# Performance work log

Hardware: AMD Instinct MI355X
Metric: run time of the kernel (lower is better)

Reference implementation:

```python
import jax, jax.numpy as jnp
import numpy as np
import math


def _build_lookup(S):
    # Vectorized port of build_hierarchical_index_lookup_table (static, numpy).
    L = int(math.log2(S))
    total = 2 * S - 1
    max_valid = total - 2  # root is never a neighbor
    idx = np.full((S, L), -1, dtype=np.int32)
    cmask = np.zeros((S, L), dtype=bool)
    n = np.arange(S, dtype=np.int64)
    for lvl in range(L):
        if lvl == 0:
            nn = n ^ 1
            pair = n
        else:
            pair = n // 2 + S
            nn = pair ^ 1
        valid = nn <= max_valid
        idx[:, lvl] = np.where(valid, nn.astype(np.int32), idx[:, lvl])
        cmask[:, lvl] = np.where(valid, (pair < nn) & valid, cmask[:, lvl])
        n = nn
    return jnp.asarray(idx), jnp.asarray(cmask)


def _tree_kv(k, v, levels, scale):
    # Build parent nodes bottom-up. Parent K is the mean of its two children;
    # parent V is refined by the fused parent-self attention (build_parent_nodes):
    # 3-way softmax over [self, child0, child1] with eps 1e-9 in the denominator.
    K_parts, V_parts = [k], [v]
    Kc, Vc = k, v
    for _ in range(levels):
        Kc0, Kc1 = Kc[:, 0::2], Kc[:, 1::2]
        Vc0, Vc1 = Vc[:, 0::2], Vc[:, 1::2]
        Kp = 0.5 * (Kc0 + Kc1)
        Vp = 0.5 * (Vc0 + Vc1)
        s_self = jnp.einsum('bphd,bphd->bph', Kp, Kp) * scale
        s0 = jnp.einsum('bphd,bphd->bph', Kp, Kc0) * scale
        s1 = jnp.einsum('bphd,bphd->bph', Kp, Kc1) * scale
        m = jnp.maximum(s_self, jnp.maximum(s0, s1))
        e_self = jnp.exp(s_self - m)
        e0 = jnp.exp(s0 - m)
        e1 = jnp.exp(s1 - m)
        denom = e_self + e0 + e1 + 1e-9
        Vp = (e_self[..., None] * Vp + e0[..., None] * Vc0 + e1[..., None] * Vc1) / denom[..., None]
        K_parts.append(Kp)
        V_parts.append(Vp)
        Kc, Vc = Kp, Vp
    # Full tree: leaves first, then each parent level -> [B, 2S-1, H, D]
    return jnp.concatenate(K_parts, axis=1), jnp.concatenate(V_parts, axis=1)


def setup_inputs() -> dict:
    key = jax.random.key(0)
    kq, kk, kv = jax.random.split(key, 3)
    B, S, H, D = 4, 4096, 8, 64
    q = jax.random.normal(kq, (B, S, H, D), dtype=jnp.float32)
    k = jax.random.normal(kk, (B, S, H, D), dtype=jnp.float32)
    v = jax.random.normal(kv, (B, S, H, D), dtype=jnp.float32)
    return {'q': q, 'k': k, 'v': v}


def reference(q, k, v):
    B, S, H, D = q.shape
    L = int(math.log2(S))
    scale = 1.0 / math.sqrt(D)
    idx, cmask = _build_lookup(S)          # [S, L] int32, [S, L] bool
    Kf, Vf = _tree_kv(k, v, L, scale)      # [B, 2S-1, H, D]
    kc = Kf[:, idx]                        # [B, S, L, H, D] tree-indexed gather
    vc = Vf[:, idx]
    s_self = jnp.einsum('bshd,bshd->bsh', q, k) * scale
    s_cross = jnp.einsum('bshd,bslhd->bshl', q, kc) * scale
    s_cross = jnp.where(cmask[None, :, None, :], -jnp.inf, s_cross)
    m = jnp.maximum(s_self, jnp.max(s_cross, axis=-1))  # online-softmax max
    e_self = jnp.exp(s_self - m)
    e_cross = jnp.exp(s_cross - m[..., None])
    denom = e_self + jnp.sum(e_cross, axis=-1)
    out = (e_self[..., None] * v + jnp.einsum('bshl,bslhd->bshd', e_cross, vc)) / denom[..., None]
    return out
```

## Files before the change

### kernel.cpp

```cpp
#include <hip/hip_runtime.h>


#define S 4096
#define H 8
#define D 64
#define B 4
#define NINT 4094
#define NBH 32
#define SCALE 0.125f

__device__ inline float red16(float x) {
    x += __shfl_xor(x, 1);
    x += __shfl_xor(x, 2);
    x += __shfl_xor(x, 4);
    x += __shfl_xor(x, 8);
    return x;
}

__device__ inline float dot4(const float4 a, const float4 b) {
    return a.x * b.x + a.y * b.y + a.z * b.z + a.w * b.w;
}

__device__ inline void combine(const float4 k0, const float4 k1,
                               const float4 v0, const float4 v1,
                               float4& kp, float4& vp) {
    kp.x = 0.5f * (k0.x + k1.x);
    kp.y = 0.5f * (k0.y + k1.y);
    kp.z = 0.5f * (k0.z + k1.z);
    kp.w = 0.5f * (k0.w + k1.w);
    float pss = red16(dot4(kp, kp)) * SCALE;
    float p0  = red16(dot4(kp, k0)) * SCALE;
    float p1  = red16(dot4(kp, k1)) * SCALE;
    float m  = fmaxf(pss, fmaxf(p0, p1));
    float es = __expf(pss - m), e0 = __expf(p0 - m), e1 = __expf(p1 - m);
    float inv = 1.0f / (es + e0 + e1 + 1e-9f);
    float h = 0.5f * es;
    vp.x = ((h + e0) * v0.x + (h + e1) * v1.x) * inv;
    vp.y = ((h + e0) * v0.y + (h + e1) * v1.y) * inv;
    vp.z = ((h + e0) * v0.z + (h + e1) * v1.z) * inv;
    vp.w = ((h + e0) * v0.w + (h + e1) * v1.w) * inv;
}

__global__ __launch_bounds__(256) void tree_chunk(
    const float* __restrict__ k, const float* __restrict__ v,
    float* __restrict__ kt, float* __restrict__ vt)
{
    __shared__ float lkA[32 * 64], lvA[32 * 64];
    __shared__ float lkB[16 * 64], lvB[16 * 64];
    const int t = threadIdx.x;
    const int sub = t & 15;
    const int pg = t >> 4;
    const int blk = blockIdx.x;
    const int c = blk & 63;
    const int bh = blk >> 6;
    const int b = bh >> 3, h = bh & 7;

#pragma unroll
    for (int r = 0; r < 2; ++r) {
        int j = pg + r * 16;
        int s0 = c * 64 + 2 * j;
        size_t a0 = ((((size_t)b * S + s0) * H + h) * D) + sub * 4;
        float4 k0 = *(const float4*)(k + a0);
        float4 k1 = *(const float4*)(k + a0 + H * D);
        float4 v0 = *(const float4*)(v + a0);
        float4 v1 = *(const float4*)(v + a0 + H * D);
        float4 kp, vp;
        combine(k0, k1, v0, v1, kp, vp);
        *(float4*)(lkA + j * 64 + sub * 4) = kp;
        *(float4*)(lvA + j * 64 + sub * 4) = vp;
        size_t g = ((size_t)bh * NINT + c * 32 + j) * 64 + sub * 4;
        *(float4*)(kt + g) = kp;
        *(float4*)(vt + g) = vp;
    }
    __syncthreads();

    float *sk = lkA, *sv = lvA, *dk = lkB, *dv = lvB;
#pragma unroll
    for (int l = 2; l <= 6; ++l) {
        int np = 64 >> l;
        int goff = S - (S >> (l - 1));
        if (pg < np) {
            int j = pg;
            float4 k0 = *(const float4*)(sk + (2 * j) * 64 + sub * 4);
            float4 k1 = *(const float4*)(sk + (2 * j + 1) * 64 + sub * 4);
            float4 v0 = *(const float4*)(sv + (2 * j) * 64 + sub * 4);
            float4 v1 = *(const float4*)(sv + (2 * j + 1) * 64 + sub * 4);
            float4 kp, vp;
            combine(k0, k1, v0, v1, kp, vp);
            if (l < 6) {
                *(float4*)(dk + j * 64 + sub * 4) = kp;
                *(float4*)(dv + j * 64 + sub * 4) = vp;
            }
            size_t g = ((size_t)bh * NINT + goff + c * np + j) * 64 + sub * 4;
            *(float4*)(kt + g) = kp;
            *(float4*)(vt + g) = vp;
        }
        __syncthreads();
        float* tp;
        tp = sk; sk = dk; dk = tp;
        tp = sv; sv = dv; dv = tp;
    }
}

__global__ __launch_bounds__(256) void tree_top(
    float* __restrict__ kt, float* __restrict__ vt)
{
    __shared__ float lkA[64 * 64], lvA[64 * 64];
    __shared__ float lkB[32 * 64], lvB[32 * 64];
    const int t = threadIdx.x;
    const int sub = t & 15;
    const int pg = t >> 4;
    const int bh = blockIdx.x;

    for (int i = t; i < 1024; i += 256) {
        size_t g = ((size_t)bh * NINT + 3968) * 64 + i * 4;
        *(float4*)(lkA + i * 4) = *(const float4*)(kt + g);
        *(float4*)(lvA + i * 4) = *(const float4*)(vt + g);
    }
    __syncthreads();

    float *sk = lkA, *sv = lvA, *dk = lkB, *dv = lvB;
    int cn = 64;
#pragma unroll
    for (int l = 7; l <= 11; ++l) {
        int np = cn >> 1;
        int goff = S - (S >> (l - 1));
        for (int j = pg; j < np; j += 16) {
            float4 k0 = *(const float4*)(sk + (2 * j) * 64 + sub * 4);
            float4 k1 = *(const float4*)(sk + (2 * j + 1) * 64 + sub * 4);
            float4 v0 = *(const float4*)(sv + (2 * j) * 64 + sub * 4);
            float4 v1 = *(const float4*)(sv + (2 * j + 1) * 64 + sub * 4);
            float4 kp, vp;
            combine(k0, k1, v0, v1, kp, vp);
            if (l < 11) {
                *(float4*)(dk + j * 64 + sub * 4) = kp;
                *(float4*)(dv + j * 64 + sub * 4) = vp;
            }
            size_t g = ((size_t)bh * NINT + goff + j) * 64 + sub * 4;
            *(float4*)(kt + g) = kp;
            *(float4*)(vt + g) = vp;
        }
        __syncthreads();
        float* tp;
        tp = sk; sk = dk; dk = tp;
        tp = sv; sv = dv; dv = tp;
        cn = np;
    }
}

__global__ __launch_bounds__(256) void attn(
    const float* __restrict__ q, const float* __restrict__ k,
    const float* __restrict__ v,
    const float* __restrict__ kt, const float* __restrict__ vt,
    float* __restrict__ out)
{
    int t = blockIdx.x * 256 + threadIdx.x;
    int lane = t & 63;
    int sub = lane & 15;
    int qi = lane >> 4;
    int w = t >> 6;
    int hg = w & 1;
    int s = (w >> 1) & (S - 1);
    int b = w >> 13;
    int h = hg * 4 + qi;
    int bh = b * 8 + h;
    size_t qa = ((((size_t)b * S + s) * H + h) * D) + sub * 4;

    float4 q4 = *(const float4*)(q + qa);
    float4 k4 = *(const float4*)(k + qa);
    float4 v4 = *(const float4*)(v + qa);

    float4 kc[12], vc[12];
    size_t tb = (size_t)bh * NINT;
#pragma unroll
    for (int l = 0; l < 12; ++l) {
        if ((s >> l) & 1) {
            if (l == 0) {
                kc[0] = *(const float4*)(k + qa - H * D);
                vc[0] = *(const float4*)(v + qa - H * D);
            } else {
                int node = (S - (S >> (l - 1))) + ((s >> l) ^ 1);
                size_t a = (tb + node) * 64 + sub * 4;
                kc[l] = *(const float4*)(kt + a);
                vc[l] = *(const float4*)(vt + a);
            }
        }
    }

    float ss = red16(dot4(q4, k4)) * SCALE;
    float sc[12];
#pragma unroll
    for (int l = 0; l < 12; ++l) {
        if ((s >> l) & 1) sc[l] = red16(dot4(q4, kc[l])) * SCALE;
        else              sc[l] = -1e38f;
    }

    float m = ss;
#pragma unroll
    for (int l = 0; l < 12; ++l) m = fmaxf(m, sc[l]);

    float es = __expf(ss - m);
    float denom = es;
    float4 acc;
    acc.x = es * v4.x; acc.y = es * v4.y; acc.z = es * v4.z; acc.w = es * v4.w;
#pragma unroll
    for (int l = 0; l < 12; ++l) {
        if ((s >> l) & 1) {
            float e = __expf(sc[l] - m);
            denom += e;
            acc.x += e * vc[l].x;
            acc.y += e * vc[l].y;
            acc.z += e * vc[l].z;
            acc.w += e * vc[l].w;
        }
    }
    float inv = 1.0f / denom;
    float4 o;
    o.x = acc.x * inv; o.y = acc.y * inv; o.z = acc.z * inv; o.w = acc.w * inv;
    *(float4*)(out + qa) = o;
}

extern "C" void kernel_launch(void* const* d_in, const int* in_sizes, int n_in,
                              void* d_out, int out_size, void* d_ws, size_t ws_size,
                              hipStream_t stream) {
    const float* q = (const float*)d_in[0];
    const float* k = (const float*)d_in[1];
    const float* v = (const float*)d_in[2];
    float* outp = (float*)d_out;
    float* kt = (float*)d_ws;
    float* vt = kt + (size_t)NBH * NINT * D;

    hipLaunchKernelGGL(tree_chunk, dim3(NBH * 64), dim3(256), 0, stream,
                       k, v, kt, vt);
    hipLaunchKernelGGL(tree_top, dim3(NBH), dim3(256), 0, stream, kt, vt);
    hipLaunchKernelGGL(attn, dim3((B * S * 2 * 64) / 256), dim3(256), 0, stream,
                       q, k, v, kt, vt, outp);
}
```

Measured before the change: 177.0 us.

## Recompute low tree levels in attention chunks, store only upper levels globally

```diff
diff --git a/kernel.cpp b/kernel.cpp
--- a/kernel.cpp
+++ b/kernel.cpp
@@ -5,8 +5,8 @@
 #define H 8
 #define D 64
 #define B 4
-#define NINT 4094
 #define NBH 32
+#define NHI 126
 #define SCALE 0.125f
 
 __device__ inline float red16(float x) {
@@ -41,9 +41,9 @@
     vp.w = ((h + e0) * v0.w + (h + e1) * v1.w) * inv;
 }
 
-__global__ __launch_bounds__(256) void tree_chunk(
+__global__ __launch_bounds__(256) void chunk_root(
     const float* __restrict__ k, const float* __restrict__ v,
-    float* __restrict__ kt, float* __restrict__ vt)
+    float* __restrict__ khi, float* __restrict__ vhi)
 {
     __shared__ float lkA[32 * 64], lvA[32 * 64];
     __shared__ float lkB[16 * 64], lvB[16 * 64];
@@ -68,9 +68,6 @@
         combine(k0, k1, v0, v1, kp, vp);
         *(float4*)(lkA + j * 64 + sub * 4) = kp;
         *(float4*)(lvA + j * 64 + sub * 4) = vp;
-        size_t g = ((size_t)bh * NINT + c * 32 + j) * 64 + sub * 4;
-        *(float4*)(kt + g) = kp;
-        *(float4*)(vt + g) = vp;
     }
     __syncthreads();
 
@@ -78,7 +75,6 @@
 #pragma unroll
     for (int l = 2; l <= 6; ++l) {
         int np = 64 >> l;
-        int goff = S - (S >> (l - 1));
         if (pg < np) {
             int j = pg;
             float4 k0 = *(const float4*)(sk + (2 * j) * 64 + sub * 4);
@@ -90,10 +86,11 @@
             if (l < 6) {
                 *(float4*)(dk + j * 64 + sub * 4) = kp;
                 *(float4*)(dv + j * 64 + sub * 4) = vp;
-            }
-            size_t g = ((size_t)bh * NINT + goff + c * np + j) * 64 + sub * 4;
-            *(float4*)(kt + g) = kp;
-            *(float4*)(vt + g) = vp;
+            } else {
+                size_t g = ((size_t)bh * NHI + c) * 64 + sub * 4;
+                *(float4*)(khi + g) = kp;
+                *(float4*)(vhi + g) = vp;
+            }
         }
         __syncthreads();
         float* tp;
@@ -102,122 +99,186 @@
     }
 }
 
-__global__ __launch_bounds__(256) void tree_top(
-    float* __restrict__ kt, float* __restrict__ vt)
+__global__ __launch_bounds__(256) void build_hi(
+    float* __restrict__ khi, float* __restrict__ vhi)
 {
-    __shared__ float lkA[64 * 64], lvA[64 * 64];
-    __shared__ float lkB[32 * 64], lvB[32 * 64];
+    __shared__ float lk[NHI * 64], lv[NHI * 64];
     const int t = threadIdx.x;
     const int sub = t & 15;
     const int pg = t >> 4;
     const int bh = blockIdx.x;
+    size_t base = (size_t)bh * NHI * 64;
 
     for (int i = t; i < 1024; i += 256) {
-        size_t g = ((size_t)bh * NINT + 3968) * 64 + i * 4;
-        *(float4*)(lkA + i * 4) = *(const float4*)(kt + g);
-        *(float4*)(lvA + i * 4) = *(const float4*)(vt + g);
+        *(float4*)(lk + i * 4) = *(const float4*)(khi + base + i * 4);
+        *(float4*)(lv + i * 4) = *(const float4*)(vhi + base + i * 4);
     }
     __syncthreads();
 
-    float *sk = lkA, *sv = lvA, *dk = lkB, *dv = lvB;
-    int cn = 64;
+    int srcOff = 0, dstOff = 64, np = 32;
 #pragma unroll
     for (int l = 7; l <= 11; ++l) {
-        int np = cn >> 1;
-        int goff = S - (S >> (l - 1));
         for (int j = pg; j < np; j += 16) {
-            float4 k0 = *(const float4*)(sk + (2 * j) * 64 + sub * 4);
-            float4 k1 = *(const float4*)(sk + (2 * j + 1) * 64 + sub * 4);
-            float4 v0 = *(const float4*)(sv + (2 * j) * 64 + sub * 4);
-            float4 v1 = *(const float4*)(sv + (2 * j + 1) * 64 + sub * 4);
+            float4 k0 = *(const float4*)(lk + (srcOff + 2 * j) * 64 + sub * 4);
+            float4 k1 = *(const float4*)(lk + (srcOff + 2 * j + 1) * 64 + sub * 4);
+            float4 v0 = *(const float4*)(lv + (srcOff + 2 * j) * 64 + sub * 4);
+            float4 v1 = *(const float4*)(lv + (srcOff + 2 * j + 1) * 64 + sub * 4);
             float4 kp, vp;
             combine(k0, k1, v0, v1, kp, vp);
-            if (l < 11) {
-                *(float4*)(dk + j * 64 + sub * 4) = kp;
-                *(float4*)(dv + j * 64 + sub * 4) = vp;
-            }
-            size_t g = ((size_t)bh * NINT + goff + j) * 64 + sub * 4;
-            *(float4*)(kt + g) = kp;
-            *(float4*)(vt + g) = vp;
+            *(float4*)(lk + (dstOff + j) * 64 + sub * 4) = kp;
+            *(float4*)(lv + (dstOff + j) * 64 + sub * 4) = vp;
+            *(float4*)(khi + base + (size_t)(dstOff + j) * 64 + sub * 4) = kp;
+            *(float4*)(vhi + base + (size_t)(dstOff + j) * 64 + sub * 4) = vp;
         }
         __syncthreads();
-        float* tp;
-        tp = sk; sk = dk; dk = tp;
-        tp = sv; sv = dv; dv = tp;
-        cn = np;
-    }
-}
-
-__global__ __launch_bounds__(256) void attn(
+        srcOff = dstOff; dstOff += np; np >>= 1;
+    }
+}
+
+__global__ __launch_bounds__(256) void attn_chunk(
     const float* __restrict__ q, const float* __restrict__ k,
     const float* __restrict__ v,
-    const float* __restrict__ kt, const float* __restrict__ vt,
+    const float* __restrict__ khi, const float* __restrict__ vhi,
     float* __restrict__ out)
 {
-    int t = blockIdx.x * 256 + threadIdx.x;
-    int lane = t & 63;
-    int sub = lane & 15;
-    int qi = lane >> 4;
-    int w = t >> 6;
-    int hg = w & 1;
-    int s = (w >> 1) & (S - 1);
-    int b = w >> 13;
-    int h = hg * 4 + qi;
-    int bh = b * 8 + h;
-    size_t qa = ((((size_t)b * S + s) * H + h) * D) + sub * 4;
-
-    float4 q4 = *(const float4*)(q + qa);
-    float4 k4 = *(const float4*)(k + qa);
-    float4 v4 = *(const float4*)(v + qa);
-
-    float4 kc[12], vc[12];
-    size_t tb = (size_t)bh * NINT;
-#pragma unroll
-    for (int l = 0; l < 12; ++l) {
-        if ((s >> l) & 1) {
-            if (l == 0) {
-                kc[0] = *(const float4*)(k + qa - H * D);
-                vc[0] = *(const float4*)(v + qa - H * D);
-            } else {
-                int node = (S - (S >> (l - 1))) + ((s >> l) ^ 1);
-                size_t a = (tb + node) * 64 + sub * 4;
-                kc[l] = *(const float4*)(kt + a);
-                vc[l] = *(const float4*)(vt + a);
-            }
-        }
-    }
-
-    float ss = red16(dot4(q4, k4)) * SCALE;
-    float sc[12];
-#pragma unroll
-    for (int l = 0; l < 12; ++l) {
-        if ((s >> l) & 1) sc[l] = red16(dot4(q4, kc[l])) * SCALE;
-        else              sc[l] = -1e38f;
-    }
-
-    float m = ss;
-#pragma unroll
-    for (int l = 0; l < 12; ++l) m = fmaxf(m, sc[l]);
-
-    float es = __expf(ss - m);
-    float denom = es;
-    float4 acc;
-    acc.x = es * v4.x; acc.y = es * v4.y; acc.z = es * v4.z; acc.w = es * v4.w;
-#pragma unroll
-    for (int l = 0; l < 12; ++l) {
-        if ((s >> l) & 1) {
-            float e = __expf(sc[l] - m);
+    __shared__ float tk[62 * 64], tv[62 * 64];
+    __shared__ float pk[6 * 64], pv[6 * 64];
+    const int t = threadIdx.x;
+    const int sub = t & 15;
+    const int pg = t >> 4;
+    const int blk = blockIdx.x;
+    const int c = blk & 63;
+    const int bh = blk >> 6;
+    const int b = bh >> 3, h = bh & 7;
+
+    if (pg < 12) {
+        int lh = (pg >= 6) ? pg - 6 : pg;
+        if ((c >> lh) & 1) {
+            int off = 128 - (128 >> lh);
+            int node = off + ((c >> lh) ^ 1);
+            size_t a = ((size_t)bh * NHI + node) * 64 + sub * 4;
+            if (pg < 6) *(float4*)(pk + lh * 64 + sub * 4) = *(const float4*)(khi + a);
+            else        *(float4*)(pv + lh * 64 + sub * 4) = *(const float4*)(vhi + a);
+        }
+    }
+
+#pragma unroll
+    for (int r = 0; r < 2; ++r) {
+        int j = pg + r * 16;
+        int s0 = c * 64 + 2 * j;
+        size_t a0 = ((((size_t)b * S + s0) * H + h) * D) + sub * 4;
+        float4 k0 = *(const float4*)(k + a0);
+        float4 k1 = *(const float4*)(k + a0 + H * D);
+        float4 v0 = *(const float4*)(v + a0);
+        float4 v1 = *(const float4*)(v + a0 + H * D);
+        float4 kp, vp;
+        combine(k0, k1, v0, v1, kp, vp);
+        *(float4*)(tk + j * 64 + sub * 4) = kp;
+        *(float4*)(tv + j * 64 + sub * 4) = vp;
+    }
+    __syncthreads();
+
+    {
+        int srcOff = 0, dstOff = 32, np = 16;
+#pragma unroll
+        for (int l = 2; l <= 5; ++l) {
+            if (pg < np) {
+                int j = pg;
+                float4 k0 = *(const float4*)(tk + (srcOff + 2 * j) * 64 + sub * 4);
+                float4 k1 = *(const float4*)(tk + (srcOff + 2 * j + 1) * 64 + sub * 4);
+                float4 v0 = *(const float4*)(tv + (srcOff + 2 * j) * 64 + sub * 4);
+                float4 v1 = *(const float4*)(tv + (srcOff + 2 * j + 1) * 64 + sub * 4);
+                float4 kp, vp;
+                combine(k0, k1, v0, v1, kp, vp);
+                *(float4*)(tk + (dstOff + j) * 64 + sub * 4) = kp;
+                *(float4*)(tv + (dstOff + j) * 64 + sub * 4) = vp;
+            }
+            __syncthreads();
+            srcOff = dstOff; dstOff += np; np >>= 1;
+        }
+    }
+
+#pragma unroll 1
+    for (int r = 0; r < 4; ++r) {
+        int sl = pg + r * 16;
+        int s = c * 64 + sl;
+        size_t qa = ((((size_t)b * S + s) * H + h) * D) + sub * 4;
+        float4 q4 = *(const float4*)(q + qa);
+        float4 k4 = *(const float4*)(k + qa);
+        float4 v4 = *(const float4*)(v + qa);
+
+        float ss = red16(dot4(q4, k4)) * SCALE;
+
+        float sc[12];
+        float4 vc0 = v4;
+        const bool odd = (s & 1) != 0;
+        if (odd) {
+            float4 kc0 = *(const float4*)(k + qa - H * D);
+            vc0 = *(const float4*)(v + qa - H * D);
+            sc[0] = red16(dot4(q4, kc0)) * SCALE;
+        } else {
+            sc[0] = -1e38f;
+        }
+#pragma unroll
+        for (int l = 1; l <= 5; ++l) {
+            if ((s >> l) & 1) {
+                int base = 64 - (64 >> (l - 1));
+                int loc = base + (((s >> l) ^ 1) - (c << (6 - l)));
+                float4 kc = *(const float4*)(tk + loc * 64 + sub * 4);
+                sc[l] = red16(dot4(q4, kc)) * SCALE;
+            } else sc[l] = -1e38f;
+        }
+#pragma unroll
+        for (int l = 6; l <= 11; ++l) {
+            if ((c >> (l - 6)) & 1) {
+                float4 kc = *(const float4*)(pk + (l - 6) * 64 + sub * 4);
+                sc[l] = red16(dot4(q4, kc)) * SCALE;
+            } else sc[l] = -1e38f;
+        }
+
+        float m = ss;
+#pragma unroll
+        for (int l = 0; l < 12; ++l) m = fmaxf(m, sc[l]);
+
+        float es = __expf(ss - m);
+        float denom = es;
+        float4 acc;
+        acc.x = es * v4.x; acc.y = es * v4.y; acc.z = es * v4.z; acc.w = es * v4.w;
+
+        if (odd) {
+            float e = __expf(sc[0] - m);
             denom += e;
-            acc.x += e * vc[l].x;
-            acc.y += e * vc[l].y;
-            acc.z += e * vc[l].z;
-            acc.w += e * vc[l].w;
-        }
-    }
-    float inv = 1.0f / denom;
-    float4 o;
-    o.x = acc.x * inv; o.y = acc.y * inv; o.z = acc.z * inv; o.w = acc.w * inv;
-    *(float4*)(out + qa) = o;
+            acc.x += e * vc0.x; acc.y += e * vc0.y;
+            acc.z += e * vc0.z; acc.w += e * vc0.w;
+        }
+#pragma unroll
+        for (int l = 1; l <= 5; ++l) {
+            if ((s >> l) & 1) {
+                int base = 64 - (64 >> (l - 1));
+                int loc = base + (((s >> l) ^ 1) - (c << (6 - l)));
+                float4 vc = *(const float4*)(tv + loc * 64 + sub * 4);
+                float e = __expf(sc[l] - m);
+                denom += e;
+                acc.x += e * vc.x; acc.y += e * vc.y;
+                acc.z += e * vc.z; acc.w += e * vc.w;
+            }
+        }
+#pragma unroll
+        for (int l = 6; l <= 11; ++l) {
+            if ((c >> (l - 6)) & 1) {
+                float4 vc = *(const float4*)(pv + (l - 6) * 64 + sub * 4);
+                float e = __expf(sc[l] - m);
+                denom += e;
+                acc.x += e * vc.x; acc.y += e * vc.y;
+                acc.z += e * vc.z; acc.w += e * vc.w;
+            }
+        }
+        float inv = 1.0f / denom;
+        float4 o;
+        o.x = acc.x * inv; o.y = acc.y * inv;
+        o.z = acc.z * inv; o.w = acc.w * inv;
+        *(float4*)(out + qa) = o;
+    }
 }
 
 extern "C" void kernel_launch(void* const* d_in, const int* in_sizes, int n_in,
@@ -227,12 +288,12 @@
     const float* k = (const float*)d_in[1];
     const float* v = (const float*)d_in[2];
     float* outp = (float*)d_out;
-    float* kt = (float*)d_ws;
-    float* vt = kt + (size_t)NBH * NINT * D;
-
-    hipLaunchKernelGGL(tree_chunk, dim3(NBH * 64), dim3(256), 0, stream,
-                       k, v, kt, vt);
-    hipLaunchKernelGGL(tree_top, dim3(NBH), dim3(256), 0, stream, kt, vt);
-    hipLaunchKernelGGL(attn, dim3((B * S * 2 * 64) / 256), dim3(256), 0, stream,
-                       q, k, v, kt, vt, outp);
-}
+    float* khi = (float*)d_ws;
+    float* vhi = khi + (size_t)NBH * NHI * D;
+
+    hipLaunchKernelGGL(chunk_root, dim3(NBH * 64), dim3(256), 0, stream,
+                       k, v, khi, vhi);
+    hipLaunchKernelGGL(build_hi, dim3(NBH), dim3(256), 0, stream, khi, vhi);
+    hipLaunchKernelGGL(attn_chunk, dim3(NBH * 64), dim3(256), 0, stream,
+                       q, k, v, khi, vhi, outp);
+}
```

Measured after the change: 168.3 us. -4.9%, faster.
